# Kernel tuning notes

Hardware: AMD Instinct MI355X
Metric: run time of the kernel (lower is better)

## Reference

```python
import jax, jax.numpy as jnp
import numpy as np

N_HEAD = 32
N_KV_HEAD = 8
ROPE_THETA = 500000.0


def rotate_half(x):
    d = x.shape[-1] // 2
    return jnp.concatenate((-x[..., d:], x[..., :d]), axis=-1)


def setup_inputs() -> dict:
    key = jax.random.key(0)
    ks = jax.random.split(key, 5)
    C = 2048
    B, T = 2, 2048
    s = 1.0 / np.sqrt(C)
    return {
        "x": jax.random.normal(ks[0], (B, T, C), dtype=jnp.float32),
        "Wq": jax.random.normal(ks[1], (C, C), dtype=jnp.float32) * s,
        "Wk": jax.random.normal(ks[2], (C, 512), dtype=jnp.float32) * s,
        "Wv": jax.random.normal(ks[3], (C, 512), dtype=jnp.float32) * s,
        "Wo": jax.random.normal(ks[4], (C, C), dtype=jnp.float32) * s,
    }


def reference(x, Wq, Wk, Wv, Wo):
    B, T, C = x.shape
    H, KV = N_HEAD, N_KV_HEAD
    D = C // H
    n_rep = H // KV

    q = (x @ Wq).reshape(B, T, H, D).transpose(0, 2, 1, 3)   # [B,H,T,D]
    k = (x @ Wk).reshape(B, T, KV, D).transpose(0, 2, 1, 3)  # [B,KV,T,D]
    v = (x @ Wv).reshape(B, T, KV, D).transpose(0, 2, 1, 3)  # [B,KV,T,D]

    # RoPE: cos/sin of shape [1,1,T,D], broadcast over batch and heads
    inv_freq = 1.0 / (ROPE_THETA ** (jnp.arange(0, D, 2, dtype=jnp.float32) / D))
    freqs = jnp.arange(T, dtype=jnp.float32)[:, None] * inv_freq[None, :]  # [T,D/2]
    emb = jnp.concatenate((freqs, freqs), axis=-1)  # [T,D]
    cos = jnp.cos(emb)[None, None].astype(x.dtype)
    sin = jnp.sin(emb)[None, None].astype(x.dtype)

    q = q * cos + rotate_half(q) * sin
    k = k * cos + rotate_half(k) * sin

    # repeat_kv (GQA expansion): [B,KV,T,D] -> [B,H,T,D]
    k = jnp.repeat(k, n_rep, axis=1)
    v = jnp.repeat(v, n_rep, axis=1)

    scale = 1.0 / jnp.sqrt(jnp.asarray(D, dtype=x.dtype))
    scores = jnp.einsum("bhqd,bhkd->bhqk", q, k) * scale  # [B,H,T,T]
    causal = jnp.tril(jnp.ones((T, T), dtype=bool))
    scores = jnp.where(causal[None, None], scores, jnp.finfo(scores.dtype).min)
    attn = jax.nn.softmax(scores, axis=-1)
    y = jnp.einsum("bhqk,bhkd->bhqd", attn, v)  # [B,H,T,D]
    y = y.transpose(0, 2, 1, 3).reshape(B, T, C)
    return y @ Wo
```

## Files before the change

### kernel.cpp

```cpp
#include <hip/hip_runtime.h>

using u16 = unsigned short;
using u32 = unsigned int;

typedef __attribute__((ext_vector_type(8))) __bf16 bf16x8;
typedef __attribute__((ext_vector_type(4))) float f32x4;
typedef __attribute__((ext_vector_type(16))) float f32x16;

#define DEVI __device__ __forceinline__

DEVI float bf2f(u16 u) {
  union { u32 i; float f; } v; v.i = ((u32)u) << 16; return v.f;
}
DEVI u16 f2bf(float f) {
  union { float f; u32 u; } v; v.f = f;
  u32 u = v.u;
  u32 r = (u + 0x7fffu + ((u >> 16) & 1u)) >> 16;
  return (u16)r;
}
DEVI u32 pkbf(float a, float b) {
  union { __bf16 h[2]; u32 u; } t;
  t.h[0] = (__bf16)a; t.h[1] = (__bf16)b;
  return t.u;
}

DEVI void gload16(const u16* g, u16* l) {
  __builtin_amdgcn_global_load_lds(
      (const __attribute__((address_space(1))) void*)g,
      (__attribute__((address_space(3))) void*)l, 16, 0, 0);
}

__global__ __launch_bounds__(256) void cvt_bf16_f32(const float* __restrict__ in,
                                                    u16* __restrict__ out, int n8) {
  int i = blockIdx.x * 256 + threadIdx.x;
  if (i >= n8) return;
  const float4* fin = (const float4*)in;
  float4 a = fin[i * 2], b = fin[i * 2 + 1];
  u16 o[8] = {f2bf(a.x), f2bf(a.y), f2bf(a.z), f2bf(a.w),
              f2bf(b.x), f2bf(b.y), f2bf(b.z), f2bf(b.w)};
  ((uint4*)out)[i] = *(const uint4*)o;
}

DEVI void tcvt64_body(const float* in, u16* out, int R, int Cc, int c0, int r0, int t,
                      u16 (*tile)[72]) {
  {
    int row = t >> 2, part = t & 3;
    const float* src = in + (size_t)(r0 + row) * Cc + c0 + part * 16;
    float4 f0 = ((const float4*)src)[0];
    float4 f1 = ((const float4*)src)[1];
    float4 f2 = ((const float4*)src)[2];
    float4 f3 = ((const float4*)src)[3];
    u16 v[16] = {f2bf(f0.x), f2bf(f0.y), f2bf(f0.z), f2bf(f0.w),
                 f2bf(f1.x), f2bf(f1.y), f2bf(f1.z), f2bf(f1.w),
                 f2bf(f2.x), f2bf(f2.y), f2bf(f2.z), f2bf(f2.w),
                 f2bf(f3.x), f2bf(f3.y), f2bf(f3.z), f2bf(f3.w)};
    *(uint4*)&tile[row][part * 16]     = ((const uint4*)v)[0];
    *(uint4*)&tile[row][part * 16 + 8] = ((const uint4*)v)[1];
  }
  __syncthreads();
  {
    int c = t & 63, rq = t >> 6;
    u16 v[16];
#pragma unroll
    for (int i = 0; i < 16; i++) v[i] = tile[rq * 16 + i][c];
    u16* dst = out + (size_t)(c0 + c) * R + r0 + rq * 16;
    ((uint4*)dst)[0] = ((const uint4*)v)[0];
    ((uint4*)dst)[1] = ((const uint4*)v)[1];
  }
}

__global__ __launch_bounds__(256) void transpose_cvt64(const float* __restrict__ in,
                                                       u16* __restrict__ out,
                                                       int R, int Cc) {
  __shared__ u16 tile[64][72];
  tcvt64_body(in, out, R, Cc, blockIdx.x * 64, blockIdx.y * 64, threadIdx.x, tile);
}

__global__ __launch_bounds__(256) void transpose_wqkv(const float* __restrict__ Wq,
                                                      const float* __restrict__ Wk,
                                                      const float* __restrict__ Wv,
                                                      u16* __restrict__ out) {
  __shared__ u16 tile[64][72];
  int bx = blockIdx.x;
  const float* in;
  u16* dst;
  int Cc, c0;
  if (bx < 32)      { in = Wq; dst = out;                        Cc = 2048; c0 = bx * 64; }
  else if (bx < 40) { in = Wk; dst = out + (size_t)2048 * 2048;  Cc = 512;  c0 = (bx - 32) * 64; }
  else              { in = Wv; dst = out + (size_t)2560 * 2048;  Cc = 512;  c0 = (bx - 40) * 64; }
  tcvt64_body(in, dst, 2048, Cc, c0, blockIdx.y * 64, threadIdx.x, tile);
}

__global__ __launch_bounds__(256) void transpose_sl64(const u16* __restrict__ in, int ldin,
                                                      u16* __restrict__ out,
                                                      int R, int Cc) {
  __shared__ u16 tile[64][72];
  int c0 = blockIdx.x * 64, r0 = blockIdx.y * 64;
  int t = threadIdx.x;
  {
    int row = t >> 2, part = t & 3;
    const u16* src = in + (size_t)(r0 + row) * ldin + c0 + part * 16;
    uint4 a = ((const uint4*)src)[0];
    uint4 b = ((const uint4*)src)[1];
    *(uint4*)&tile[row][part * 16]     = a;
    *(uint4*)&tile[row][part * 16 + 8] = b;
  }
  __syncthreads();
  {
    int c = t & 63, rq = t >> 6;
    u16 v[16];
#pragma unroll
    for (int i = 0; i < 16; i++) v[i] = tile[rq * 16 + i][c];
    u16* dst = out + (size_t)(c0 + c) * R + r0 + rq * 16;
    ((uint4*)dst)[0] = ((const uint4*)v)[0];
    ((uint4*)dst)[1] = ((const uint4*)v)[1];
  }
}

DEVI void rope_body(u16* X, int h4shift, float scale, int idx) {
  int hq   = idx & ((1 << h4shift) - 1);
  int row  = idx >> h4shift;
  int head = hq >> 2;
  int d0   = (hq & 3) * 8;
  int tpos = row & 2047;
  size_t base = (size_t)row * 3072 + head * 64 + d0;
  uint4 lo = *(const uint4*)(X + base);
  uint4 hi = *(const uint4*)(X + base + 32);
  const u16* lp = (const u16*)&lo;
  const u16* hp = (const u16*)&hi;
  float ang = (float)tpos * exp2f(-(float)d0 * 0.59161152f);
  u16 o0[8], o1[8];
#pragma unroll
  for (int i = 0; i < 8; i++) {
    float s, c;
    __sincosf(ang, &s, &c);
    s *= scale; c *= scale;
    float x0 = bf2f(lp[i]);
    float x1 = bf2f(hp[i]);
    o0[i] = f2bf(x0 * c - x1 * s);
    o1[i] = f2bf(x1 * c + x0 * s);
    ang *= 0.6636011f;
  }
  *(uint4*)(X + base)      = *(const uint4*)o0;
  *(uint4*)(X + base + 32) = *(const uint4*)o1;
}

__global__ __launch_bounds__(256) void rope_fused(u16* __restrict__ QKV) {
  const int NQ = 4096 * 128;
  int idx = blockIdx.x * 256 + threadIdx.x;
  if (idx < NQ) rope_body(QKV, 7, 0.18033688f, idx);
  else          rope_body(QKV + 2048, 5, 1.0f, idx - NQ);
}

DEVI void cstore(u16* C, size_t idx, float v)   { C[idx] = f2bf(v); }
DEVI void cstore(float* C, size_t idx, float v) { C[idx] = v; }

template <typename TO>
__global__ __launch_bounds__(256) void gemm128(const u16* __restrict__ A,
                                               const u16* __restrict__ Bt,
                                               TO* __restrict__ C,
                                               int M, int N, int K) {
  __shared__ u16 As[2 * 128 * 32];
  __shared__ u16 Bs[2 * 128 * 32];
  int tid = threadIdx.x, wid = tid >> 6, lane = tid & 63;
  int quad = lane >> 4, l15 = lane & 15;
  int m0 = blockIdx.y * 128, n0 = blockIdx.x * 128;
  int wm = (wid >> 1) * 64, wn = (wid & 1) * 64;

  int r0s = wid * 16 + (lane >> 2);
  int r1s = 64 + wid * 16 + (lane >> 2);
  int cblk = lane & 3;
  int cs0 = (cblk ^ ((r0s >> 1) & 3)) * 8;
  int cs1 = (cblk ^ ((r1s >> 1) & 3)) * 8;
  u16* lA0 = As + wid * 512 + lane * 8;
  u16* lA1 = As + (4 + wid) * 512 + lane * 8;
  u16* lB0 = Bs + wid * 512 + lane * 8;
  u16* lB1 = Bs + (4 + wid) * 512 + lane * 8;
  const u16* gA0 = A + (size_t)(m0 + r0s) * K + cs0;
  const u16* gA1 = A + (size_t)(m0 + r1s) * K + cs1;
  const u16* gB0 = Bt + (size_t)(n0 + r0s) * K + cs0;
  const u16* gB1 = Bt + (size_t)(n0 + r1s) * K + cs1;

  f32x4 acc[4][4];
  for (int i = 0; i < 4; i++)
    for (int j = 0; j < 4; j++) acc[i][j] = f32x4{0.f, 0.f, 0.f, 0.f};

  gload16(gA0, lA0);
  gload16(gA1, lA1);
  gload16(gB0, lB0);
  gload16(gB1, lB1);
  __builtin_amdgcn_s_waitcnt(0x0F70);
  __syncthreads();

  int cur = 0;
  for (int k0 = 0; k0 < K; k0 += 32) {
    int nb = cur ^ 1;
    if (k0 + 32 < K) {
      gload16(gA0 + k0 + 32, lA0 + nb * 4096);
      gload16(gA1 + k0 + 32, lA1 + nb * 4096);
      gload16(gB0 + k0 + 32, lB0 + nb * 4096);
      gload16(gB1 + k0 + 32, lB1 + nb * 4096);
    }
    const u16* Ab = As + cur * 4096;
    const u16* Bb = Bs + cur * 4096;
    bf16x8 af[4], bf_[4];
    for (int mi = 0; mi < 4; mi++) {
      int row = wm + mi * 16 + l15;
      af[mi] = *(const bf16x8*)(Ab + row * 32 + ((quad ^ ((row >> 1) & 3)) * 8));
    }
    for (int ni = 0; ni < 4; ni++) {
      int row = wn + ni * 16 + l15;
      bf_[ni] = *(const bf16x8*)(Bb + row * 32 + ((quad ^ ((row >> 1) & 3)) * 8));
    }
    for (int mi = 0; mi < 4; mi++)
      for (int ni = 0; ni < 4; ni++)
        acc[mi][ni] = __builtin_amdgcn_mfma_f32_16x16x32_bf16(af[mi], bf_[ni], acc[mi][ni], 0, 0, 0);
    __builtin_amdgcn_s_waitcnt(0x0F70);
    __syncthreads();
    cur = nb;
  }
  for (int mi = 0; mi < 4; mi++)
    for (int ni = 0; ni < 4; ni++)
      for (int r = 0; r < 4; r++) {
        int row = m0 + wm + mi * 16 + quad * 4 + r;
        int col = n0 + wn + ni * 16 + l15;
        cstore(C, (size_t)row * N + col, acc[mi][ni][r]);
      }
}

__global__ __launch_bounds__(256) void attn64(const u16* __restrict__ QKV,
                                              const u16* __restrict__ Vt,
                                              u16* __restrict__ Y) {
  __shared__ u16 Ks[2 * 64 * 64];
  __shared__ u16 Vst[2 * 64 * 64];

  int tid = threadIdx.x, wid = tid >> 6, lane = tid & 63;
  int l31 = lane & 31, hi = lane >> 5;
  int bh = blockIdx.y, b = bh >> 5, h = bh & 31, kvh = h >> 2;
  int p = blockIdx.x;

  int kr  = wid * 8 + (lane >> 3);
  int kgn = lane & 7;
  const u16* gK0 = QKV + (size_t)(b * 2048 + kr) * 3072 + 2048 + kvh * 64
                 + ((kgn ^ (kr & 7)) * 8);
  u16* lK0 = Ks + wid * 512 + lane * 8;

  int vr = tid >> 3, vg = tid & 7;
  const u16* gV0 = Vt + (size_t)(kvh * 64 + vr) * 4096 + b * 2048 + vg * 8;
  u16* lV0 = Vst + vr * 64 + ((vg ^ (vr & 7)) * 8);

  f32x16 fzero;
#pragma unroll
  for (int i = 0; i < 16; i++) fzero[i] = 0.f;
  bf16x8 onesf;
  {
    union { u16 w[8]; bf16x8 v; } t;
#pragma unroll
    for (int i = 0; i < 8; i++) t.w[i] = 0x3F80;
    onesf = t.v;
  }

  for (int pass = 0; pass < 2; pass++) {
    int j   = pass ? (15 - p) : p;
    int q0w = j * 128 + wid * 32;
    int qg  = q0w + l31;

    bf16x8 qf[4];
    {
      const u16* qp = QKV + (size_t)(b * 2048 + qg) * 3072 + h * 64 + hi * 8;
#pragma unroll
      for (int dh = 0; dh < 4; dh++) qf[dh] = *(const bf16x8*)(qp + dh * 16);
    }

    f32x16 o0, o1, zacc;
#pragma unroll
    for (int i = 0; i < 16; i++) { o0[i] = 0.f; o1[i] = 0.f; zacc[i] = 0.f; }

    int nkt = 2 * (j + 1);

    {
      uint4 va = *(const uint4*)(gV0);
      uint4 vb = *(const uint4*)(gV0 + 32 * 4096);
      gload16(gK0, lK0);
      gload16(gK0 + 32 * 3072, lK0 + 2048);
      __builtin_amdgcn_s_waitcnt(0x0F70);
      *(uint4*)(lV0)        = va;
      *(uint4*)(lV0 + 2048) = vb;
    }
    __syncthreads();

    int cur = 0;
    for (int kt = 0; kt < nkt; kt++) {
      int kbase = kt * 64;
      int nxt = cur ^ 1;
      bool more = (kt + 1 < nkt);
      uint4 va, vb;
      if (more) {
        size_t ko = (size_t)(kbase + 64);
        va = *(const uint4*)(gV0 + ko);
        vb = *(const uint4*)(gV0 + 32 * 4096 + ko);
        gload16(gK0 + ko * 3072, lK0 + nxt * 4096);
        gload16(gK0 + ko * 3072 + 32 * 3072, lK0 + nxt * 4096 + 2048);
      }

      const u16* Kb = Ks + cur * 4096;
      const u16* Vb = Vst + cur * 4096;
#pragma unroll
      for (int sub = 0; sub < 2; sub++) {
        int kb = kbase + sub * 32;
        if (kb > q0w) break;

        bf16x8 kf0 = *(const bf16x8*)(Kb + (sub * 32 + l31) * 64 + (((0 * 2 + hi) ^ (l31 & 7)) * 8));
        f32x16 s = __builtin_amdgcn_mfma_f32_32x32x16_bf16(kf0, qf[0], fzero, 0, 0, 0);
#pragma unroll
        for (int dh = 1; dh < 4; dh++) {
          int g = (dh * 2 + hi) ^ (l31 & 7);
          bf16x8 kf = *(const bf16x8*)(Kb + (sub * 32 + l31) * 64 + g * 8);
          s = __builtin_amdgcn_mfma_f32_32x32x16_bf16(kf, qf[dh], s, 0, 0, 0);
        }

        float pb[16];
        if (kb < q0w) {
#pragma unroll
          for (int r = 0; r < 16; r++) pb[r] = exp2f(s[r]);
        } else {
#pragma unroll
          for (int r = 0; r < 16; r++) {
            int key = kb + (r & 3) + 8 * (r >> 2) + 4 * hi;
            pb[r] = (key <= qg) ? exp2f(s[r]) : 0.f;
          }
        }

#pragma unroll
        for (int kk = 0; kk < 2; kk++) {
          const float* pp = pb + kk * 8;
          u32 a01 = pkbf(pp[0], pp[1]);
          u32 a23 = pkbf(pp[2], pp[3]);
          u32 a45 = pkbf(pp[4], pp[5]);
          u32 a67 = pkbf(pp[6], pp[7]);
          asm volatile("v_permlane32_swap_b32 %0, %1" : "+v"(a01), "+v"(a45));
          asm volatile("v_permlane32_swap_b32 %0, %1" : "+v"(a23), "+v"(a67));
          union { u32 w[4]; bf16x8 v; } pf;
          pf.w[0] = a01; pf.w[1] = a23; pf.w[2] = a45; pf.w[3] = a67;
          int kgr = sub * 4 + kk * 2 + hi;
          const u16* vp = Vb + l31 * 64 + ((kgr ^ (l31 & 7)) * 8);
          bf16x8 v0 = *(const bf16x8*)(vp);
          bf16x8 v1 = *(const bf16x8*)(vp + 2048);
          zacc = __builtin_amdgcn_mfma_f32_32x32x16_bf16(pf.v, onesf, zacc, 0, 0, 0);
          o0 = __builtin_amdgcn_mfma_f32_32x32x16_bf16(pf.v, v0, o0, 0, 0, 0);
          o1 = __builtin_amdgcn_mfma_f32_32x32x16_bf16(pf.v, v1, o1, 0, 0, 0);
        }
      }

      if (more) {
        __builtin_amdgcn_s_waitcnt(0x0F70);
        *(uint4*)(lV0 + nxt * 4096)        = va;
        *(uint4*)(lV0 + nxt * 4096 + 2048) = vb;
      }
      __syncthreads();
      cur = nxt;
    }

#pragma unroll
    for (int r = 0; r < 16; r++) {
      int qr = (r & 3) + 8 * (r >> 2) + 4 * hi;
      float inv = 1.f / zacc[r];
      size_t row = (size_t)(b * 2048 + q0w + qr);
      Y[row * 2048 + h * 64 + l31]      = f2bf(o0[r] * inv);
      Y[row * 2048 + h * 64 + 32 + l31] = f2bf(o1[r] * inv);
    }
  }
}

extern "C" void kernel_launch(void* const* d_in, const int* in_sizes, int n_in,
                              void* d_out, int out_size, void* d_ws, size_t ws_size,
                              hipStream_t stream) {
  const float* x  = (const float*)d_in[0];
  const float* Wq = (const float*)d_in[1];
  const float* Wk = (const float*)d_in[2];
  const float* Wv = (const float*)d_in[3];
  const float* Wo = (const float*)d_in[4];
  float* outp = (float*)d_out;

  u16* xb    = (u16*)d_ws;
  u16* WqkvT = xb + 8388608;
  u16* QKV   = WqkvT + 6291456;
  u16* Vt    = QKV + 12582912;
  u16* Yb    = xb;
  u16* WoT   = WqkvT;

  cvt_bf16_f32<<<4096, 256, 0, stream>>>(x, xb, 1048576);

  transpose_wqkv<<<dim3(48, 32), 256, 0, stream>>>(Wq, Wk, Wv, WqkvT);

  gemm128<u16><<<dim3(24, 32), 256, 0, stream>>>(xb, WqkvT, QKV, 4096, 3072, 2048);

  rope_fused<<<2560, 256, 0, stream>>>(QKV);

  transpose_sl64<<<dim3(8, 64), 256, 0, stream>>>(QKV + 2560, 3072, Vt, 4096, 512);

  attn64<<<dim3(8, 64), 256, 0, stream>>>(QKV, Vt, Yb);

  transpose_cvt64<<<dim3(32, 32), 256, 0, stream>>>(Wo, WoT, 2048, 2048);
  gemm128<float><<<dim3(16, 32), 256, 0, stream>>>(Yb, WoT, outp, 4096, 2048, 2048);
}
```

Measured before the change: 322.5 us.

## Split paired attention passes into separate blocks and replace ones-MFMA row sum

The attention kernel previously paired a short and a long causal query tile in one block over two passes. It now launches one block per query tile, giving twice as many blocks, with the largest tiles dispatched first. The softmax denominator is no longer computed by an extra MFMA against a ones vector. Each lane now sums the fp32 probabilities as it goes, and the sums are combined with lane shuffles at the end. This removes a third of the PV-stage MFMAs and lets the hardware scheduler balance the causal workload, at the cost of extra block launches and Q loads, plus a small mismatch between the bf16-rounded probabilities used for O and the fp32 sums used for normalisation.

```diff
diff --git a/kernel.cpp b/kernel.cpp
--- a/kernel.cpp
+++ b/kernel.cpp
@@ -237,7 +237,7 @@
   int tid = threadIdx.x, wid = tid >> 6, lane = tid & 63;
   int l31 = lane & 31, hi = lane >> 5;
   int bh = blockIdx.y, b = bh >> 5, h = bh & 31, kvh = h >> 2;
-  int p = blockIdx.x;
+  int j = 15 - blockIdx.x;
 
   int kr  = wid * 8 + (lane >> 3);
   int kgn = lane & 7;
@@ -252,123 +252,122 @@
   f32x16 fzero;
 #pragma unroll
   for (int i = 0; i < 16; i++) fzero[i] = 0.f;
-  bf16x8 onesf;
-  {
-    union { u16 w[8]; bf16x8 v; } t;
-#pragma unroll
-    for (int i = 0; i < 8; i++) t.w[i] = 0x3F80;
-    onesf = t.v;
-  }
-
-  for (int pass = 0; pass < 2; pass++) {
-    int j   = pass ? (15 - p) : p;
-    int q0w = j * 128 + wid * 32;
-    int qg  = q0w + l31;
-
-    bf16x8 qf[4];
-    {
-      const u16* qp = QKV + (size_t)(b * 2048 + qg) * 3072 + h * 64 + hi * 8;
-#pragma unroll
-      for (int dh = 0; dh < 4; dh++) qf[dh] = *(const bf16x8*)(qp + dh * 16);
-    }
-
-    f32x16 o0, o1, zacc;
-#pragma unroll
-    for (int i = 0; i < 16; i++) { o0[i] = 0.f; o1[i] = 0.f; zacc[i] = 0.f; }
-
-    int nkt = 2 * (j + 1);
-
-    {
-      uint4 va = *(const uint4*)(gV0);
-      uint4 vb = *(const uint4*)(gV0 + 32 * 4096);
-      gload16(gK0, lK0);
-      gload16(gK0 + 32 * 3072, lK0 + 2048);
-      __builtin_amdgcn_s_waitcnt(0x0F70);
-      *(uint4*)(lV0)        = va;
-      *(uint4*)(lV0 + 2048) = vb;
-    }
-    __syncthreads();
-
-    int cur = 0;
-    for (int kt = 0; kt < nkt; kt++) {
-      int kbase = kt * 64;
-      int nxt = cur ^ 1;
-      bool more = (kt + 1 < nkt);
-      uint4 va, vb;
-      if (more) {
-        size_t ko = (size_t)(kbase + 64);
-        va = *(const uint4*)(gV0 + ko);
-        vb = *(const uint4*)(gV0 + 32 * 4096 + ko);
-        gload16(gK0 + ko * 3072, lK0 + nxt * 4096);
-        gload16(gK0 + ko * 3072 + 32 * 3072, lK0 + nxt * 4096 + 2048);
+
+  int q0w = j * 128 + wid * 32;
+  int qg  = q0w + l31;
+
+  bf16x8 qf[4];
+  {
+    const u16* qp = QKV + (size_t)(b * 2048 + qg) * 3072 + h * 64 + hi * 8;
+#pragma unroll
+    for (int dh = 0; dh < 4; dh++) qf[dh] = *(const bf16x8*)(qp + dh * 16);
+  }
+
+  f32x16 o0, o1;
+#pragma unroll
+  for (int i = 0; i < 16; i++) { o0[i] = 0.f; o1[i] = 0.f; }
+  float zsum = 0.f;
+
+  int nkt = 2 * (j + 1);
+
+  {
+    uint4 va = *(const uint4*)(gV0);
+    uint4 vb = *(const uint4*)(gV0 + 32 * 4096);
+    gload16(gK0, lK0);
+    gload16(gK0 + 32 * 3072, lK0 + 2048);
+    __builtin_amdgcn_s_waitcnt(0x0F70);
+    *(uint4*)(lV0)        = va;
+    *(uint4*)(lV0 + 2048) = vb;
+  }
+  __syncthreads();
+
+  int cur = 0;
+  for (int kt = 0; kt < nkt; kt++) {
+    int kbase = kt * 64;
+    int nxt = cur ^ 1;
+    bool more = (kt + 1 < nkt);
+    uint4 va, vb;
+    if (more) {
+      size_t ko = (size_t)(kbase + 64);
+      va = *(const uint4*)(gV0 + ko);
+      vb = *(const uint4*)(gV0 + 32 * 4096 + ko);
+      gload16(gK0 + ko * 3072, lK0 + nxt * 4096);
+      gload16(gK0 + ko * 3072 + 32 * 3072, lK0 + nxt * 4096 + 2048);
+    }
+
+    const u16* Kb = Ks + cur * 4096;
+    const u16* Vb = Vst + cur * 4096;
+#pragma unroll
+    for (int sub = 0; sub < 2; sub++) {
+      int kb = kbase + sub * 32;
+      if (kb > q0w) break;
+
+      bf16x8 kf0 = *(const bf16x8*)(Kb + (sub * 32 + l31) * 64 + ((hi ^ (l31 & 7)) * 8));
+      f32x16 s = __builtin_amdgcn_mfma_f32_32x32x16_bf16(kf0, qf[0], fzero, 0, 0, 0);
+#pragma unroll
+      for (int dh = 1; dh < 4; dh++) {
+        int g = (dh * 2 + hi) ^ (l31 & 7);
+        bf16x8 kf = *(const bf16x8*)(Kb + (sub * 32 + l31) * 64 + g * 8);
+        s = __builtin_amdgcn_mfma_f32_32x32x16_bf16(kf, qf[dh], s, 0, 0, 0);
       }
 
-      const u16* Kb = Ks + cur * 4096;
-      const u16* Vb = Vst + cur * 4096;
-#pragma unroll
-      for (int sub = 0; sub < 2; sub++) {
-        int kb = kbase + sub * 32;
-        if (kb > q0w) break;
-
-        bf16x8 kf0 = *(const bf16x8*)(Kb + (sub * 32 + l31) * 64 + (((0 * 2 + hi) ^ (l31 & 7)) * 8));
-        f32x16 s = __builtin_amdgcn_mfma_f32_32x32x16_bf16(kf0, qf[0], fzero, 0, 0, 0);
-#pragma unroll
-        for (int dh = 1; dh < 4; dh++) {
-          int g = (dh * 2 + hi) ^ (l31 & 7);
-          bf16x8 kf = *(const bf16x8*)(Kb + (sub * 32 + l31) * 64 + g * 8);
-          s = __builtin_amdgcn_mfma_f32_32x32x16_bf16(kf, qf[dh], s, 0, 0, 0);
+      float pb[16];
+      if (kb < q0w) {
+#pragma unroll
+        for (int r = 0; r < 16; r++) {
+          float pv = exp2f(s[r]);
+          zsum += pv;
+          pb[r] = pv;
         }
-
-        float pb[16];
-        if (kb < q0w) {
-#pragma unroll
-          for (int r = 0; r < 16; r++) pb[r] = exp2f(s[r]);
-        } else {
-#pragma unroll
-          for (int r = 0; r < 16; r++) {
-            int key = kb + (r & 3) + 8 * (r >> 2) + 4 * hi;
-            pb[r] = (key <= qg) ? exp2f(s[r]) : 0.f;
-          }
-        }
-
-#pragma unroll
-        for (int kk = 0; kk < 2; kk++) {
-          const float* pp = pb + kk * 8;
-          u32 a01 = pkbf(pp[0], pp[1]);
-          u32 a23 = pkbf(pp[2], pp[3]);
-          u32 a45 = pkbf(pp[4], pp[5]);
-          u32 a67 = pkbf(pp[6], pp[7]);
-          asm volatile("v_permlane32_swap_b32 %0, %1" : "+v"(a01), "+v"(a45));
-          asm volatile("v_permlane32_swap_b32 %0, %1" : "+v"(a23), "+v"(a67));
-          union { u32 w[4]; bf16x8 v; } pf;
-          pf.w[0] = a01; pf.w[1] = a23; pf.w[2] = a45; pf.w[3] = a67;
-          int kgr = sub * 4 + kk * 2 + hi;
-          const u16* vp = Vb + l31 * 64 + ((kgr ^ (l31 & 7)) * 8);
-          bf16x8 v0 = *(const bf16x8*)(vp);
-          bf16x8 v1 = *(const bf16x8*)(vp + 2048);
-          zacc = __builtin_amdgcn_mfma_f32_32x32x16_bf16(pf.v, onesf, zacc, 0, 0, 0);
-          o0 = __builtin_amdgcn_mfma_f32_32x32x16_bf16(pf.v, v0, o0, 0, 0, 0);
-          o1 = __builtin_amdgcn_mfma_f32_32x32x16_bf16(pf.v, v1, o1, 0, 0, 0);
+      } else {
+#pragma unroll
+        for (int r = 0; r < 16; r++) {
+          int key = kb + (r & 3) + 8 * (r >> 2) + 4 * hi;
+          float pv = (key <= qg) ? exp2f(s[r]) : 0.f;
+          zsum += pv;
+          pb[r] = pv;
         }
       }
 
-      if (more) {
-        __builtin_amdgcn_s_waitcnt(0x0F70);
-        *(uint4*)(lV0 + nxt * 4096)        = va;
-        *(uint4*)(lV0 + nxt * 4096 + 2048) = vb;
+#pragma unroll
+      for (int kk = 0; kk < 2; kk++) {
+        const float* pp = pb + kk * 8;
+        u32 a01 = pkbf(pp[0], pp[1]);
+        u32 a23 = pkbf(pp[2], pp[3]);
+        u32 a45 = pkbf(pp[4], pp[5]);
+        u32 a67 = pkbf(pp[6], pp[7]);
+        asm volatile("v_permlane32_swap_b32 %0, %1" : "+v"(a01), "+v"(a45));
+        asm volatile("v_permlane32_swap_b32 %0, %1" : "+v"(a23), "+v"(a67));
+        union { u32 w[4]; bf16x8 v; } pf;
+        pf.w[0] = a01; pf.w[1] = a23; pf.w[2] = a45; pf.w[3] = a67;
+        int kgr = sub * 4 + kk * 2 + hi;
+        const u16* vp = Vb + l31 * 64 + ((kgr ^ (l31 & 7)) * 8);
+        bf16x8 v0 = *(const bf16x8*)(vp);
+        bf16x8 v1 = *(const bf16x8*)(vp + 2048);
+        o0 = __builtin_amdgcn_mfma_f32_32x32x16_bf16(pf.v, v0, o0, 0, 0, 0);
+        o1 = __builtin_amdgcn_mfma_f32_32x32x16_bf16(pf.v, v1, o1, 0, 0, 0);
       }
-      __syncthreads();
-      cur = nxt;
-    }
-
-#pragma unroll
-    for (int r = 0; r < 16; r++) {
-      int qr = (r & 3) + 8 * (r >> 2) + 4 * hi;
-      float inv = 1.f / zacc[r];
-      size_t row = (size_t)(b * 2048 + q0w + qr);
-      Y[row * 2048 + h * 64 + l31]      = f2bf(o0[r] * inv);
-      Y[row * 2048 + h * 64 + 32 + l31] = f2bf(o1[r] * inv);
-    }
+    }
+
+    if (more) {
+      __builtin_amdgcn_s_waitcnt(0x0F70);
+      *(uint4*)(lV0 + nxt * 4096)        = va;
+      *(uint4*)(lV0 + nxt * 4096 + 2048) = vb;
+    }
+    __syncthreads();
+    cur = nxt;
+  }
+
+  float zf = zsum + __shfl_xor(zsum, 32);
+
+#pragma unroll
+  for (int r = 0; r < 16; r++) {
+    int qr = (r & 3) + 8 * (r >> 2) + 4 * hi;
+    float zr = __shfl(zf, qr, 64);
+    float inv = 1.f / zr;
+    size_t row = (size_t)(b * 2048 + q0w + qr);
+    Y[row * 2048 + h * 64 + l31]      = f2bf(o0[r] * inv);
+    Y[row * 2048 + h * 64 + 32 + l31] = f2bf(o1[r] * inv);
   }
 }
 
@@ -399,7 +398,7 @@
 
   transpose_sl64<<<dim3(8, 64), 256, 0, stream>>>(QKV + 2560, 3072, Vt, 4096, 512);
 
-  attn64<<<dim3(8, 64), 256, 0, stream>>>(QKV, Vt, Yb);
+  attn64<<<dim3(16, 64), 256, 0, stream>>>(QKV, Vt, Yb);
 
   transpose_cvt64<<<dim3(32, 32), 256, 0, stream>>>(Wo, WoT, 2048, 2048);
   gemm128<float><<<dim3(16, 32), 256, 0, stream>>>(Yb, WoT, outp, 4096, 2048, 2048);
```

Measured after the change: 364.6 us. 1.13x slower.
